# Performance work log

Hardware: AMD Instinct MI355X
Metric: run time of the kernel (lower is better)

Reference implementation:

```python
import jax, jax.numpy as jnp
import numpy as np

KNOTS = 17

def _buffers():
    t = jnp.linspace(0.0, 3.0, KNOTS)                # (K,)
    dt = 3.0 / (KNOTS - 1)
    w = jnp.full((KNOTS,), 2.0 * dt)
    w = w.at[jnp.array([0, KNOTS - 1])].set(dt)      # trapezoid-like weights
    phi = jnp.exp(-t * t / 2.0)                      # standard normal CF
    return t, phi, w * phi


def setup_inputs() -> dict:
    key = jax.random.key(0)
    kz, ka = jax.random.split(key)
    n, d, num_proj = 8192, 768, 1024
    z = jax.random.normal(kz, (n, d), dtype=jnp.float32)
    a = jax.random.normal(ka, (d, num_proj), dtype=jnp.float32)
    return {"z": z, "a": a}


def reference(z, a):
    t, phi, weights = _buffers()
    # normalize projection directions (columns of a) to unit L2 norm
    a_n = a / jnp.linalg.norm(a, axis=0, keepdims=True)          # (d, P)
    proj = z @ a_n                                               # (n, P)
    x_t = proj[..., None] * t                                    # (n, P, K)
    cos_mean = jnp.cos(x_t).mean(axis=-3)                        # (P, K)
    sin_mean = jnp.sin(x_t).mean(axis=-3)                        # (P, K)
    err = (cos_mean - phi) ** 2 + sin_mean ** 2                  # (P, K)
    n = z.shape[-2]
    return (err @ weights * n).mean()                            # scalar
```

## Files before the change

kernel.cpp:

```cpp
#include <hip/hip_runtime.h>
#include <math.h>

typedef __attribute__((ext_vector_type(8))) short bf16x8;
typedef __attribute__((ext_vector_type(4))) float f32x4;

#define N_ROWS 8192
#define D_DIM  768
#define P_DIM  1024
#define KNOTS  17
#define NK     16
#define NCH    128
#define KSTEPS 12

__device__ inline unsigned short f2bf(float f) {
    union { float f; unsigned int u; } x; x.f = f;
    unsigned int r = x.u + 0x7FFFu + ((x.u >> 16) & 1u);
    return (unsigned short)(r >> 16);
}

__device__ inline void gload_lds16(const unsigned short* g, const unsigned short* l) {
    auto gp = reinterpret_cast<const __attribute__((address_space(1))) char*>(
        reinterpret_cast<uintptr_t>(g));
    auto lp = reinterpret_cast<__attribute__((address_space(3))) char*>(
        (uintptr_t)(unsigned int)reinterpret_cast<uintptr_t>(l));
    __builtin_amdgcn_global_load_lds(gp, lp, 16, 0, 0);
}

__global__ __launch_bounds__(256) void colsq_kernel(const float* __restrict__ a,
                                                    float* __restrict__ cpart) {
    int p  = blockIdx.x * 256 + threadIdx.x;
    int d0 = blockIdx.y * 64;
    float s = 0.f;
    for (int d = 0; d < 64; ++d) {
        float v = a[(size_t)(d0 + d) * P_DIM + p];
        s = fmaf(v, v, s);
    }
    cpart[(size_t)blockIdx.y * P_DIM + p] = s;
}

__global__ __launch_bounds__(256) void zconv_kernel(const float* __restrict__ z,
                                                    unsigned short* __restrict__ zh) {
    size_t i = ((size_t)blockIdx.x * 256 + threadIdx.x) * 4;
    float4 v = *reinterpret_cast<const float4*>(z + i);
    ushort4 o;
    o.x = f2bf(v.x); o.y = f2bf(v.y); o.z = f2bf(v.z); o.w = f2bf(v.w);
    *reinterpret_cast<ushort4*>(zh + i) = o;
}

__global__ __launch_bounds__(256) void atconv_kernel(const float* __restrict__ a,
                                                     const float* __restrict__ cpart,
                                                     unsigned short* __restrict__ Bt) {
    __shared__ float tile[64][65];
    __shared__ float linv[64];
    const int d0 = blockIdx.x * 64, p0 = blockIdx.y * 64;
    const int tid = threadIdx.x;
    if (tid < 64) {
        float s = 0.f;
        #pragma unroll
        for (int j = 0; j < D_DIM / 64; ++j)
            s += cpart[(size_t)j * P_DIM + p0 + tid];
        linv[tid] = rsqrtf(s);
    }
    #pragma unroll
    for (int pass = 0; pass < 16; ++pass) {
        int idx = pass * 256 + tid;
        int dr = idx >> 6, pc = idx & 63;
        tile[dr][pc] = a[(size_t)(d0 + dr) * P_DIM + p0 + pc];
    }
    __syncthreads();
    #pragma unroll
    for (int pass = 0; pass < 16; ++pass) {
        int idx = pass * 256 + tid;
        int pr = idx >> 6, dc = idx & 63;
        Bt[(size_t)(p0 + pr) * D_DIM + d0 + dc] = f2bf(tile[dc][pr] * linv[pr]);
    }
}

__global__ __launch_bounds__(512, 4) void gemmcf_kernel(const unsigned short* __restrict__ A,
                                                        const unsigned short* __restrict__ B,
                                                        float* __restrict__ part) {
    __shared__ unsigned short AsB[2][128 * 64];
    __shared__ unsigned short BsB[2][128 * 64];
    const int tid  = threadIdx.x;
    const int lane = tid & 63;
    const int wave = tid >> 6;
    const int wr = wave >> 2, wc = wave & 3;

    const int bid = blockIdx.x + blockIdx.y * 8;
    const int swz = (bid & 7) * 64 + (bid >> 3);
    const int bx = swz & 7, by = swz >> 3;
    const int row0 = by * 128;
    const int col0 = bx * 128;

    const int srow = wave * 16 + (lane >> 3);
    const int sc   = (lane & 7) ^ ((lane >> 3) & 7);
    const unsigned short* Ag = A + (size_t)(row0 + srow) * D_DIM + sc * 8;
    const unsigned short* Bg = B + (size_t)(col0 + srow) * D_DIM + sc * 8;
    const int ldsw = wave * 16 * 64;

#define STAGE(kt, db)  do { const int k0_ = (kt) * 64;                       \
        gload_lds16(Ag + k0_,             &AsB[db][ldsw]);                   \
        gload_lds16(Ag + k0_ + 8 * D_DIM, &AsB[db][ldsw + 8 * 64]);          \
        gload_lds16(Bg + k0_,             &BsB[db][ldsw]);                   \
        gload_lds16(Bg + k0_ + 8 * D_DIM, &BsB[db][ldsw + 8 * 64]); } while (0)

    f32x4 acc[4][2] = {};

    STAGE(0, 0);
    #pragma unroll
    for (int t = 0; t < KSTEPS; ++t) {
        const int cur = t & 1;
        if (t + 1 < KSTEPS) {
            STAGE(t + 1, cur ^ 1);
            asm volatile("s_waitcnt vmcnt(4)" ::: "memory");
        } else {
            asm volatile("s_waitcnt vmcnt(0)" ::: "memory");
        }
        __builtin_amdgcn_sched_barrier(0);
        __builtin_amdgcn_s_barrier();
        #pragma unroll
        for (int kk = 0; kk < 2; ++kk) {
            bf16x8 af[4], bfr[2];
            const int kg = kk * 4 + (lane >> 4);
            const int kph = (kg ^ (lane & 7)) * 8;
            #pragma unroll
            for (int mi = 0; mi < 4; ++mi)
                af[mi] = *reinterpret_cast<const bf16x8*>(
                    &AsB[cur][(wr * 64 + mi * 16 + (lane & 15)) * 64 + kph]);
            #pragma unroll
            for (int ni = 0; ni < 2; ++ni)
                bfr[ni] = *reinterpret_cast<const bf16x8*>(
                    &BsB[cur][(wc * 32 + ni * 16 + (lane & 15)) * 64 + kph]);
            #pragma unroll
            for (int mi = 0; mi < 4; ++mi)
                #pragma unroll
                for (int ni = 0; ni < 2; ++ni)
                    acc[mi][ni] = __builtin_amdgcn_mfma_f32_16x16x32_bf16(
                        af[mi], bfr[ni], acc[mi][ni], 0, 0, 0);
        }
        __builtin_amdgcn_s_barrier();
    }
#undef STAGE

    const float dt = 0.1875f;
    #pragma unroll
    for (int ni = 0; ni < 2; ++ni) {
        float cs[NK], ss[NK];
        #pragma unroll
        for (int k = 0; k < NK; ++k) { cs[k] = 0.f; ss[k] = 0.f; }
        #pragma unroll
        for (int mi = 0; mi < 4; ++mi)
            #pragma unroll
            for (int j = 0; j < 4; ++j) {
                float th = acc[mi][ni][j] * dt;
                float s1 = __sinf(th);
                float c1 = __cosf(th);
                float c2 = 2.f * c1;
                float ckm2 = 1.f, skm2 = 0.f;
                float ckm1 = c1,  skm1 = s1;
                cs[0] += c1; ss[0] += s1;
                #pragma unroll
                for (int k = 2; k <= NK; ++k) {
                    float ck = fmaf(c2, ckm1, -ckm2);
                    float sk = fmaf(c2, skm1, -skm2);
                    cs[k - 1] += ck; ss[k - 1] += sk;
                    ckm2 = ckm1; skm2 = skm1;
                    ckm1 = ck;   skm1 = sk;
                }
            }
        #pragma unroll
        for (int k = 0; k < NK; ++k) {
            cs[k] += __shfl_xor(cs[k], 16);
            cs[k] += __shfl_xor(cs[k], 32);
            ss[k] += __shfl_xor(ss[k], 16);
            ss[k] += __shfl_xor(ss[k], 32);
        }
        if (lane < 16) {
            int col = col0 + wc * 32 + ni * 16 + lane;
            size_t base = ((size_t)(by * 2 + wr) * 2 * NK) * P_DIM + col;
            #pragma unroll
            for (int k = 0; k < NK; ++k) {
                part[base + (size_t)k * P_DIM]        = cs[k];
                part[base + (size_t)(NK + k) * P_DIM] = ss[k];
            }
        }
    }
}

__global__ __launch_bounds__(256) void red1_kernel(const float* __restrict__ part,
                                                   float* __restrict__ sums) {
    int g = blockIdx.x * 256 + threadIdx.x;
    float s = 0.f;
    for (int c = 0; c < NCH; ++c)
        s += part[(size_t)c * 2 * NK * P_DIM + g];
    sums[g] = s;
}

__global__ __launch_bounds__(1024) void red2_kernel(const float* __restrict__ sums,
                                                    float* __restrict__ out) {
    const int p = threadIdx.x;
    const float dt = 0.1875f;
    const float inv_n = 1.0f / (float)N_ROWS;
    float contrib = 0.f;
    #pragma unroll
    for (int k = 1; k <= NK; ++k) {
        float cm   = sums[(k - 1) * P_DIM + p] * inv_n;
        float sm   = sums[(NK + k - 1) * P_DIM + p] * inv_n;
        float tk   = dt * (float)k;
        float phik = expf(-0.5f * tk * tk);
        float wk   = (k == KNOTS - 1) ? dt : 2.f * dt;
        float d    = cm - phik;
        contrib += wk * phik * (d * d + sm * sm);
    }
    __shared__ float red[1024];
    red[p] = contrib;
    __syncthreads();
    for (int sft = 512; sft > 0; sft >>= 1) {
        if (p < sft) red[p] += red[p + sft];
        __syncthreads();
    }
    if (p == 0) out[0] = red[0] * (float)N_ROWS / (float)P_DIM;
}

extern "C" void kernel_launch(void* const* d_in, const int* in_sizes, int n_in,
                              void* d_out, int out_size, void* d_ws, size_t ws_size,
                              hipStream_t stream) {
    const float* z = (const float*)d_in[0];
    const float* a = (const float*)d_in[1];
    float* out = (float*)d_out;

    char* ws = (char*)d_ws;
    float*          cpart = (float*)ws;
    unsigned short* zh    = (unsigned short*)(ws + 65536);
    unsigned short* Bt    = (unsigned short*)(ws + 65536 + 12582912);
    float*          part  = (float*)(ws + 65536 + 12582912 + 1572864);
    float*          sums  = (float*)(ws + 65536 + 12582912 + 1572864 + 16777216);

    colsq_kernel<<<dim3(P_DIM / 256, D_DIM / 64), 256, 0, stream>>>(a, cpart);
    zconv_kernel<<<dim3(N_ROWS * D_DIM / (256 * 4)), 256, 0, stream>>>(z, zh);
    atconv_kernel<<<dim3(D_DIM / 64, P_DIM / 64), 256, 0, stream>>>(a, cpart, Bt);
    gemmcf_kernel<<<dim3(P_DIM / 128, N_ROWS / 128), 512, 0, stream>>>(zh, Bt, part);
    red1_kernel<<<dim3(2 * NK * P_DIM / 256), 256, 0, stream>>>(part, sums);
    red2_kernel<<<1, 1024, 0, stream>>>(sums, out);
}
```

Baseline: 120.8 us.

## Fuse z fp32-to-bf16 conversion into GEMM A-tile loading

Drops the separate zconv kernel and its bf16 copy of z. The GEMM now loads fp32 z rows straight into registers, converts them to bf16 and writes them into a padded LDS tile (row stride 72), prefetching one k-step ahead. B keeps its async global-to-LDS path. This removes one launch and the write and re-read of a 12 MB intermediate. In exchange, each GEMM block reads twice as many bytes for A, which is re-read by the 8 column blocks, and it adds conversion ALU work and a full vmcnt/lgkmcnt drain at every step.

Result: no change. 119.5 us (-1.1%).

```diff
diff --git a/kernel.cpp b/kernel.cpp
--- a/kernel.cpp
+++ b/kernel.cpp
@@ -11,11 +11,19 @@
 #define NK     16
 #define NCH    128
 #define KSTEPS 12
+#define ALD    72
 
 __device__ inline unsigned short f2bf(float f) {
     union { float f; unsigned int u; } x; x.f = f;
     unsigned int r = x.u + 0x7FFFu + ((x.u >> 16) & 1u);
     return (unsigned short)(r >> 16);
+}
+
+__device__ inline bf16x8 pack8(float4 a, float4 b) {
+    union { unsigned short s[8]; bf16x8 v; } r;
+    r.s[0] = f2bf(a.x); r.s[1] = f2bf(a.y); r.s[2] = f2bf(a.z); r.s[3] = f2bf(a.w);
+    r.s[4] = f2bf(b.x); r.s[5] = f2bf(b.y); r.s[6] = f2bf(b.z); r.s[7] = f2bf(b.w);
+    return r.v;
 }
 
 __device__ inline void gload_lds16(const unsigned short* g, const unsigned short* l) {
@@ -36,15 +44,6 @@
         s = fmaf(v, v, s);
     }
     cpart[(size_t)blockIdx.y * P_DIM + p] = s;
-}
-
-__global__ __launch_bounds__(256) void zconv_kernel(const float* __restrict__ z,
-                                                    unsigned short* __restrict__ zh) {
-    size_t i = ((size_t)blockIdx.x * 256 + threadIdx.x) * 4;
-    float4 v = *reinterpret_cast<const float4*>(z + i);
-    ushort4 o;
-    o.x = f2bf(v.x); o.y = f2bf(v.y); o.z = f2bf(v.z); o.w = f2bf(v.w);
-    *reinterpret_cast<ushort4*>(zh + i) = o;
 }
 
 __global__ __launch_bounds__(256) void atconv_kernel(const float* __restrict__ a,
@@ -76,10 +75,10 @@
     }
 }
 
-__global__ __launch_bounds__(512, 4) void gemmcf_kernel(const unsigned short* __restrict__ A,
+__global__ __launch_bounds__(512, 4) void gemmcf_kernel(const float* __restrict__ Z,
                                                         const unsigned short* __restrict__ B,
                                                         float* __restrict__ part) {
-    __shared__ unsigned short AsB[2][128 * 64];
+    __shared__ unsigned short AsB[2][128 * ALD];
     __shared__ unsigned short BsB[2][128 * 64];
     const int tid  = threadIdx.x;
     const int lane = tid & 63;
@@ -92,45 +91,62 @@
     const int row0 = by * 128;
     const int col0 = bx * 128;
 
+    const int aR = wave * 16 + (lane >> 2);
+    const int ac = lane & 3;
+    const float* Zg = Z + (size_t)(row0 + aR) * D_DIM + ac * 8;
+
     const int srow = wave * 16 + (lane >> 3);
     const int sc   = (lane & 7) ^ ((lane >> 3) & 7);
-    const unsigned short* Ag = A + (size_t)(row0 + srow) * D_DIM + sc * 8;
     const unsigned short* Bg = B + (size_t)(col0 + srow) * D_DIM + sc * 8;
     const int ldsw = wave * 16 * 64;
 
-#define STAGE(kt, db)  do { const int k0_ = (kt) * 64;                       \
-        gload_lds16(Ag + k0_,             &AsB[db][ldsw]);                   \
-        gload_lds16(Ag + k0_ + 8 * D_DIM, &AsB[db][ldsw + 8 * 64]);          \
+    float4 ar0, ar1, ar2, ar3;
+
+#define ALOAD(kt) do { const float* zp_ = Zg + (kt) * 64;                    \
+        ar0 = *reinterpret_cast<const float4*>(zp_);                         \
+        ar1 = *reinterpret_cast<const float4*>(zp_ + 4);                     \
+        ar2 = *reinterpret_cast<const float4*>(zp_ + 32);                    \
+        ar3 = *reinterpret_cast<const float4*>(zp_ + 36); } while (0)
+#define AWRITE(db) do {                                                      \
+        *reinterpret_cast<bf16x8*>(&AsB[db][aR * ALD + ac * 8])       = pack8(ar0, ar1); \
+        *reinterpret_cast<bf16x8*>(&AsB[db][aR * ALD + (ac + 4) * 8]) = pack8(ar2, ar3); } while (0)
+#define BSTAGE(kt, db) do { const int k0_ = (kt) * 64;                       \
         gload_lds16(Bg + k0_,             &BsB[db][ldsw]);                   \
         gload_lds16(Bg + k0_ + 8 * D_DIM, &BsB[db][ldsw + 8 * 64]); } while (0)
+#define DRAIN_BARRIER() do {                                                 \
+        asm volatile("s_waitcnt vmcnt(0) lgkmcnt(0)" ::: "memory");          \
+        __builtin_amdgcn_sched_barrier(0);                                   \
+        __builtin_amdgcn_s_barrier(); } while (0)
 
     f32x4 acc[4][2] = {};
 
-    STAGE(0, 0);
+    ALOAD(0);
+    AWRITE(0);
+    BSTAGE(0, 0);
+    ALOAD(1);
+    DRAIN_BARRIER();
+
     #pragma unroll
     for (int t = 0; t < KSTEPS; ++t) {
         const int cur = t & 1;
         if (t + 1 < KSTEPS) {
-            STAGE(t + 1, cur ^ 1);
-            asm volatile("s_waitcnt vmcnt(4)" ::: "memory");
-        } else {
-            asm volatile("s_waitcnt vmcnt(0)" ::: "memory");
-        }
-        __builtin_amdgcn_sched_barrier(0);
-        __builtin_amdgcn_s_barrier();
+            AWRITE(cur ^ 1);
+            BSTAGE(t + 1, cur ^ 1);
+            if (t + 2 < KSTEPS) ALOAD(t + 2);
+        }
         #pragma unroll
         for (int kk = 0; kk < 2; ++kk) {
             bf16x8 af[4], bfr[2];
             const int kg = kk * 4 + (lane >> 4);
-            const int kph = (kg ^ (lane & 7)) * 8;
+            const int kbp = (kg ^ (lane & 7)) * 8;
             #pragma unroll
             for (int mi = 0; mi < 4; ++mi)
                 af[mi] = *reinterpret_cast<const bf16x8*>(
-                    &AsB[cur][(wr * 64 + mi * 16 + (lane & 15)) * 64 + kph]);
+                    &AsB[cur][(wr * 64 + mi * 16 + (lane & 15)) * ALD + kg * 8]);
             #pragma unroll
             for (int ni = 0; ni < 2; ++ni)
                 bfr[ni] = *reinterpret_cast<const bf16x8*>(
-                    &BsB[cur][(wc * 32 + ni * 16 + (lane & 15)) * 64 + kph]);
+                    &BsB[cur][(wc * 32 + ni * 16 + (lane & 15)) * 64 + kbp]);
             #pragma unroll
             for (int mi = 0; mi < 4; ++mi)
                 #pragma unroll
@@ -138,9 +154,12 @@
                     acc[mi][ni] = __builtin_amdgcn_mfma_f32_16x16x32_bf16(
                         af[mi], bfr[ni], acc[mi][ni], 0, 0, 0);
         }
-        __builtin_amdgcn_s_barrier();
-    }
-#undef STAGE
+        if (t + 1 < KSTEPS) DRAIN_BARRIER();
+    }
+#undef ALOAD
+#undef AWRITE
+#undef BSTAGE
+#undef DRAIN_BARRIER
 
     const float dt = 0.1875f;
     #pragma unroll
@@ -231,15 +250,13 @@
 
     char* ws = (char*)d_ws;
     float*          cpart = (float*)ws;
-    unsigned short* zh    = (unsigned short*)(ws + 65536);
-    unsigned short* Bt    = (unsigned short*)(ws + 65536 + 12582912);
-    float*          part  = (float*)(ws + 65536 + 12582912 + 1572864);
-    float*          sums  = (float*)(ws + 65536 + 12582912 + 1572864 + 16777216);
+    unsigned short* Bt    = (unsigned short*)(ws + 65536);
+    float*          part  = (float*)(ws + 65536 + 1572864);
+    float*          sums  = (float*)(ws + 65536 + 1572864 + 16777216);
 
     colsq_kernel<<<dim3(P_DIM / 256, D_DIM / 64), 256, 0, stream>>>(a, cpart);
-    zconv_kernel<<<dim3(N_ROWS * D_DIM / (256 * 4)), 256, 0, stream>>>(z, zh);
     atconv_kernel<<<dim3(D_DIM / 64, P_DIM / 64), 256, 0, stream>>>(a, cpart, Bt);
-    gemmcf_kernel<<<dim3(P_DIM / 128, N_ROWS / 128), 512, 0, stream>>>(zh, Bt, part);
+    gemmcf_kernel<<<dim3(P_DIM / 128, N_ROWS / 128), 512, 0, stream>>>(z, Bt, part);
     red1_kernel<<<dim3(2 * NK * P_DIM / 256), 256, 0, stream>>>(part, sums);
     red2_kernel<<<1, 1024, 0, stream>>>(sums, out);
 }
```
